# Optimization experiments

Measured on AMD Instinct MI355X. Metric: run time of the kernel, lower is better.

Reference implementation:

```python
import jax, jax.numpy as jnp
import numpy as np

N = 200000
F_IN = 165
H = 128
E = 3200000


def gcn_conv(x, edge_index, W, b):
    # x: [N, Fin], edge_index: [2, E], W: [Fin, Fout], b: [Fout]
    n = x.shape[0]
    h = x @ W  # linear transform first (PyG GCNConv)
    # add self loops
    loops = jnp.arange(n, dtype=edge_index.dtype)
    src = jnp.concatenate([edge_index[0], loops])
    dst = jnp.concatenate([edge_index[1], loops])
    # symmetric normalization: deg computed on dst (in-degree incl. self loops)
    deg = jax.ops.segment_sum(jnp.ones_like(dst, dtype=h.dtype), dst, num_segments=n)
    dinv = jnp.where(deg > 0, jax.lax.rsqrt(deg), 0.0)
    norm = dinv[src] * dinv[dst]  # [E+N]
    msgs = h[src] * norm[:, None]  # gather + scale
    out = jax.ops.segment_sum(msgs, dst, num_segments=n)  # scatter-add
    return out + b


def setup_inputs() -> dict:
    key = jax.random.key(0)
    k = jax.random.split(key, 8)
    x = jax.random.normal(k[0], (N, F_IN), dtype=jnp.float32)
    edge_index = jax.random.randint(k[1], (2, E), 0, N, dtype=jnp.int64)
    s1 = 1.0 / np.sqrt(F_IN)
    s2 = 1.0 / np.sqrt(H)
    W1 = jax.random.uniform(k[2], (F_IN, H), jnp.float32, -s1, s1)
    b1 = jnp.zeros((H,), jnp.float32)
    W2 = jax.random.uniform(k[3], (H, H), jnp.float32, -s2, s2)
    b2 = jnp.zeros((H,), jnp.float32)
    Wl = jax.random.uniform(k[4], (H, 2), jnp.float32, -s2, s2)
    bl = jax.random.uniform(k[5], (2,), jnp.float32, -s2, s2)
    return {"x": x, "edge_index": edge_index, "W1": W1, "b1": b1,
            "W2": W2, "b2": b2, "Wl": Wl, "bl": bl}


def reference(x, edge_index, W1, b1, W2, b2, Wl, bl):
    h = gcn_conv(x, edge_index, W1, b1)
    h = jax.nn.relu(h)
    # dropout p=0.3 is identity in eval mode
    h = gcn_conv(h, edge_index, W2, b2)
    h = jax.nn.relu(h)
    return h @ Wl + bl  # [N, 2]
```

## Files before the change

kernel.cpp:

```cpp
#include <hip/hip_runtime.h>
#include <hip/hip_bf16.h>

#define FIN 165
#define HID 128
#define NPB 256
#define MAXNB 784
#define CAP 4608
#define EPB 4096

typedef __attribute__((ext_vector_type(8))) short short8;
typedef __attribute__((ext_vector_type(4))) float float4v;

__device__ inline unsigned bf16rne(float v) {
    unsigned u = __float_as_uint(v);
    return (u + 0x7fffu + ((u >> 16) & 1u)) >> 16;
}

__device__ inline void bf16split(float v, short& h, short& l) {
    unsigned u = __float_as_uint(v);
    unsigned r = u + 0x7fffu + ((u >> 16) & 1u);
    h = (short)(r >> 16);
    float hf = __uint_as_float(((unsigned)(unsigned short)h) << 16);
    float lf = v - hf;
    unsigned u2 = __float_as_uint(lf);
    unsigned r2 = u2 + 0x7fffu + ((u2 >> 16) & 1u);
    l = (short)(r2 >> 16);
}

__global__ __launch_bounds__(256) void bucket_scatter(const int* __restrict__ src,
                                                      const int* __restrict__ dst,
                                                      int* __restrict__ gcur,
                                                      int2* __restrict__ bucketed,
                                                      int E, int n, int NB) {
    __shared__ int hist[MAXNB];
    __shared__ int base[MAXNB];
    __shared__ int lcur[MAXNB];
    int tid = threadIdx.x;
    long e0 = (long)blockIdx.x * EPB;
    for (int b = tid; b < NB; b += 256) { hist[b] = 0; lcur[b] = 0; }
    __syncthreads();
#pragma unroll
    for (int i = 0; i < EPB / 256; ++i) {
        long e = e0 + i * 256 + tid;
        if (e < E) {
            int d = dst[e], s = src[e];
            if ((unsigned)d < (unsigned)n && (unsigned)s < (unsigned)n)
                atomicAdd(&hist[d >> 8], 1);
        }
    }
    __syncthreads();
    for (int b = tid; b < NB; b += 256) {
        int h = hist[b];
        base[b] = h ? atomicAdd(&gcur[b * 16], h) : 0;
    }
    __syncthreads();
#pragma unroll
    for (int i = 0; i < EPB / 256; ++i) {
        long e = e0 + i * 256 + tid;
        if (e < E) {
            int d = dst[e], s = src[e];
            if ((unsigned)d < (unsigned)n && (unsigned)s < (unsigned)n) {
                int bk = d >> 8;
                int idx = base[bk] + atomicAdd(&lcur[bk], 1);
                if ((unsigned)idx < (unsigned)CAP)
                    bucketed[(size_t)bk * CAP + idx] = make_int2(s, d);
            }
        }
    }
}

__global__ __launch_bounds__(256) void bucket_scan(const int* __restrict__ gcur,
                                                   int* __restrict__ bb, int NB,
                                                   int* __restrict__ rowptr, int n) {
    __shared__ int sm[MAXNB];
    for (int b = threadIdx.x; b < NB; b += 256) sm[b] = gcur[b * 16];
    __syncthreads();
    if (threadIdx.x == 0) {
        int run = 0;
        for (int b = 0; b < NB; ++b) { int c = sm[b]; sm[b] = run; run += c; }
        bb[NB] = run;
        rowptr[n] = run;
    }
    __syncthreads();
    for (int b = threadIdx.x; b < NB; b += 256) bb[b] = sm[b];
}

__global__ __launch_bounds__(256) void build_csr(const int2* __restrict__ bucketed,
                                                 const int* __restrict__ bb,
                                                 float* __restrict__ dinv,
                                                 int* __restrict__ rowptr,
                                                 int* __restrict__ col, int n) {
    __shared__ int deg[NPB];
    __shared__ int scn[NPB];
    __shared__ int cur[NPB];
    int b = blockIdx.x, tid = threadIdx.x;
    int nb0 = b * NPB;
    int ebase = bb[b], cnt = bb[b + 1] - bb[b];
    deg[tid] = 0;
    __syncthreads();
    const int2* ep = bucketed + (size_t)b * CAP;
    for (int i = tid; i < cnt; i += 256) {
        int2 e = ep[i];
        atomicAdd(&deg[e.y - nb0], 1);
    }
    __syncthreads();
    int d = deg[tid];
    scn[tid] = d;
    __syncthreads();
    for (int off = 1; off < 256; off <<= 1) {
        int v = (tid >= off) ? scn[tid - off] : 0;
        __syncthreads();
        scn[tid] += v;
        __syncthreads();
    }
    int excl = scn[tid] - d;
    int node = nb0 + tid;
    if (node < n) {
        dinv[node] = rsqrtf((float)(d + 1));
        rowptr[node] = ebase + excl;
    }
    cur[tid] = excl;
    __syncthreads();
    for (int i = tid; i < cnt; i += 256) {
        int2 e = ep[i];
        int p = atomicAdd(&cur[e.y - nb0], 1);
        col[ebase + p] = e.x;
    }
}

__global__ __launch_bounds__(256) void wswz(const float* __restrict__ W,
                                            short8* __restrict__ out, int K, int k32) {
    int idx = blockIdx.x * 256 + threadIdx.x;
    int tot = k32 * 8 * 64;
    if (idx >= tot) return;
    int lane = idx & 63;
    int ct = (idx >> 6) & 7;
    int ks = idx >> 9;
    int col = ct * 16 + (lane & 15);
    int kb = ks * 32 + (lane >> 4) * 8;
    short8 hi, lo;
#pragma unroll
    for (int j = 0; j < 8; ++j) {
        int k = kb + j;
        float v = (k < K) ? W[k * HID + col] : 0.f;
        short h, l;
        bf16split(v, h, l);
        hi[j] = h; lo[j] = l;
    }
    out[idx] = hi;
    out[tot + idx] = lo;
}

__global__ __launch_bounds__(256) void gemm_mfma(const float* __restrict__ X,
                                                 const short8* __restrict__ Wsw,
                                                 const float* __restrict__ dinv,
                                                 unsigned* __restrict__ H2,
                                                 int n, int K, int kfull, int k32) {
    int wave = threadIdx.x >> 6, lane = threadIdx.x & 63;
    int r0 = blockIdx.x * 64 + wave * 16;
    int m = lane & 15, kph = lane >> 4;
    int row = r0 + m;
    const float* xrow = X + (size_t)row * K + kph * 8;
    const short8* Whi = Wsw;
    const short8* Wlo = Wsw + (size_t)k32 * 8 * 64;

    float4v acc[8];
#pragma unroll
    for (int ct = 0; ct < 8; ++ct) acc[ct] = (float4v){0.f, 0.f, 0.f, 0.f};

    for (int ks = 0; ks < kfull; ++ks) {
        float xv[8];
#pragma unroll
        for (int j = 0; j < 8; ++j) xv[j] = xrow[ks * 32 + j];
        short8 ah, al;
#pragma unroll
        for (int j = 0; j < 8; ++j) {
            short h, l; bf16split(xv[j], h, l);
            ah[j] = h; al[j] = l;
        }
#pragma unroll
        for (int ct = 0; ct < 8; ++ct) {
            short8 bh = Whi[(ks * 8 + ct) * 64 + lane];
            short8 bl = Wlo[(ks * 8 + ct) * 64 + lane];
            acc[ct] = __builtin_amdgcn_mfma_f32_16x16x32_bf16(ah, bh, acc[ct], 0, 0, 0);
            acc[ct] = __builtin_amdgcn_mfma_f32_16x16x32_bf16(al, bh, acc[ct], 0, 0, 0);
            acc[ct] = __builtin_amdgcn_mfma_f32_16x16x32_bf16(ah, bl, acc[ct], 0, 0, 0);
        }
    }
    if (kfull < k32) {
        int ks = kfull;
        int kb = ks * 32 + kph * 8;
        float xv[8];
#pragma unroll
        for (int j = 0; j < 8; ++j) xv[j] = (kb + j < K) ? xrow[ks * 32 + j] : 0.f;
        short8 ah, al;
#pragma unroll
        for (int j = 0; j < 8; ++j) {
            short h, l; bf16split(xv[j], h, l);
            ah[j] = h; al[j] = l;
        }
#pragma unroll
        for (int ct = 0; ct < 8; ++ct) {
            short8 bh = Whi[(ks * 8 + ct) * 64 + lane];
            short8 bl = Wlo[(ks * 8 + ct) * 64 + lane];
            acc[ct] = __builtin_amdgcn_mfma_f32_16x16x32_bf16(ah, bh, acc[ct], 0, 0, 0);
            acc[ct] = __builtin_amdgcn_mfma_f32_16x16x32_bf16(al, bh, acc[ct], 0, 0, 0);
            acc[ct] = __builtin_amdgcn_mfma_f32_16x16x32_bf16(ah, bl, acc[ct], 0, 0, 0);
        }
    }
    int ccol = lane & 15, crow = (lane >> 4) * 4;
    bool evenl = (ccol & 1) == 0;
#pragma unroll
    for (int r = 0; r < 4; ++r) {
        int gr = r0 + crow + r;
        float s = dinv[gr];
#pragma unroll
        for (int ct = 0; ct < 8; ++ct) {
            float v = acc[ct][r] * s;
            float p = __shfl_xor(v, 1);
            if (evenl) {
                unsigned u = bf16rne(v) | (bf16rne(p) << 16);
                H2[(size_t)gr * 64 + ct * 8 + (ccol >> 1)] = u;
            }
        }
    }
}

__device__ inline void bf2_unpack(unsigned u, float& f0, float& f1) {
    f0 = __uint_as_float(u << 16);
    f1 = __uint_as_float(u & 0xffff0000u);
}

__global__ __launch_bounds__(256) void agg_relu(const unsigned* __restrict__ HS2,
                                                const int* __restrict__ rowptr,
                                                const int* __restrict__ col,
                                                const float* __restrict__ dinv,
                                                const float* __restrict__ bias,
                                                float* __restrict__ Y, int n) {
    int node = blockIdx.x * 4 + (threadIdx.x >> 6);
    int lane = threadIdx.x & 63;
    if (node >= n) return;
    int start = rowptr[node], end = rowptr[node + 1];
    float2 acc;
    {
        float f0, f1;
        bf2_unpack(HS2[(size_t)node * 64 + lane], f0, f1);
        acc.x = f0; acc.y = f1;
    }
    for (int j0 = start; j0 < end; j0 += 64) {
        int cnt = min(64, end - j0);
        int cv = (j0 + lane < end) ? col[j0 + lane] : 0;
        int t = 0;
        for (; t + 8 <= cnt; t += 8) {
            unsigned uv[8];
#pragma unroll
            for (int q = 0; q < 8; ++q) {
                int c = __shfl(cv, t + q);
                uv[q] = HS2[(size_t)c * 64 + lane];
            }
#pragma unroll
            for (int q = 0; q < 8; ++q) {
                float f0, f1; bf2_unpack(uv[q], f0, f1);
                acc.x += f0; acc.y += f1;
            }
        }
        for (; t < cnt; ++t) {
            int c = __shfl(cv, t);
            float f0, f1; bf2_unpack(HS2[(size_t)c * 64 + lane], f0, f1);
            acc.x += f0; acc.y += f1;
        }
    }
    float s = dinv[node];
    float2 b = *(const float2*)&bias[2 * lane];
    float2 o;
    o.x = fmaxf(acc.x * s + b.x, 0.f);
    o.y = fmaxf(acc.y * s + b.y, 0.f);
    *(float2*)&Y[(long)node * HID + 2 * lane] = o;
}

__global__ __launch_bounds__(256) void agg_relu_head(const unsigned* __restrict__ HS2,
                                                     const int* __restrict__ rowptr,
                                                     const int* __restrict__ col,
                                                     const float* __restrict__ dinv,
                                                     const float* __restrict__ bias,
                                                     const float* __restrict__ Wl,
                                                     const float* __restrict__ bl,
                                                     float* __restrict__ out, int n) {
    int node = blockIdx.x * 4 + (threadIdx.x >> 6);
    int lane = threadIdx.x & 63;
    if (node >= n) return;
    int start = rowptr[node], end = rowptr[node + 1];
    float2 acc;
    {
        float f0, f1;
        bf2_unpack(HS2[(size_t)node * 64 + lane], f0, f1);
        acc.x = f0; acc.y = f1;
    }
    for (int j0 = start; j0 < end; j0 += 64) {
        int cnt = min(64, end - j0);
        int cv = (j0 + lane < end) ? col[j0 + lane] : 0;
        int t = 0;
        for (; t + 8 <= cnt; t += 8) {
            unsigned uv[8];
#pragma unroll
            for (int q = 0; q < 8; ++q) {
                int c = __shfl(cv, t + q);
                uv[q] = HS2[(size_t)c * 64 + lane];
            }
#pragma unroll
            for (int q = 0; q < 8; ++q) {
                float f0, f1; bf2_unpack(uv[q], f0, f1);
                acc.x += f0; acc.y += f1;
            }
        }
        for (; t < cnt; ++t) {
            int c = __shfl(cv, t);
            float f0, f1; bf2_unpack(HS2[(size_t)c * 64 + lane], f0, f1);
            acc.x += f0; acc.y += f1;
        }
    }
    float s = dinv[node];
    float2 b = *(const float2*)&bias[2 * lane];
    float vx = fmaxf(acc.x * s + b.x, 0.f);
    float vy = fmaxf(acc.y * s + b.y, 0.f);
    float4 wl = *(const float4*)&Wl[4 * lane];
    float a0 = vx * wl.x + vy * wl.z;
    float a1 = vx * wl.y + vy * wl.w;
#pragma unroll
    for (int off = 32; off > 0; off >>= 1) {
        a0 += __shfl_xor(a0, off);
        a1 += __shfl_xor(a1, off);
    }
    if (lane == 0) {
        out[node * 2 + 0] = a0 + bl[0];
        out[node * 2 + 1] = a1 + bl[1];
    }
}

extern "C" void kernel_launch(void* const* d_in, const int* in_sizes, int n_in,
                              void* d_out, int out_size, void* d_ws, size_t ws_size,
                              hipStream_t stream) {
    const float* x  = (const float*)d_in[0];
    const int*   ei = (const int*)d_in[1];
    const float* W1 = (const float*)d_in[2];
    const float* b1 = (const float*)d_in[3];
    const float* W2 = (const float*)d_in[4];
    const float* b2 = (const float*)d_in[5];
    const float* Wl = (const float*)d_in[6];
    const float* bl = (const float*)d_in[7];
    float* out = (float*)d_out;

    int n = in_sizes[0] / FIN;
    int E = in_sizes[1] / 2;
    int NB = (n + NPB - 1) / NPB;
    const int* srcp = ei;
    const int* dstp = ei + E;

    char* w = (char*)d_ws;
    auto alloc = [&](size_t bytes) {
        char* p = w;
        w += (bytes + 255) & ~(size_t)255;
        return (void*)p;
    };
    int*      gcur    = (int*)     alloc((size_t)NB * 16 * 4);
    int*      bb      = (int*)     alloc(((size_t)NB + 1) * 4);
    int*      rowptr  = (int*)     alloc(((size_t)n + 1) * 4);
    float*    dinv    = (float*)   alloc((size_t)n * 4);
    int*      colv    = (int*)     alloc((size_t)E * 4);
    unsigned* hbuf    = (unsigned*)alloc((size_t)n * 64 * 4);
    float*    ybuf    = (float*)   alloc((size_t)n * HID * 4);
    const int K32_1 = (FIN + 31) / 32;
    const int K32_2 = HID / 32;
    short8*   w1sw    = (short8*)  alloc((size_t)2 * K32_1 * 8 * 64 * 16);
    short8*   w2sw    = (short8*)  alloc((size_t)2 * K32_2 * 8 * 64 * 16);
    int2*     bucketed = (int2*)ybuf;

    hipMemsetAsync(gcur, 0, (size_t)NB * 16 * 4, stream);

    wswz<<<(K32_1 * 8 * 64 + 255) / 256, 256, 0, stream>>>(W1, w1sw, FIN, K32_1);
    wswz<<<(K32_2 * 8 * 64 + 255) / 256, 256, 0, stream>>>(W2, w2sw, HID, K32_2);

    bucket_scatter<<<(E + EPB - 1) / EPB, 256, 0, stream>>>(srcp, dstp, gcur,
                                                            bucketed, E, n, NB);
    bucket_scan<<<1, 256, 0, stream>>>(gcur, bb, NB, rowptr, n);
    build_csr<<<NB, 256, 0, stream>>>(bucketed, bb, dinv, rowptr, colv, n);

    gemm_mfma<<<n / 64, 256, 0, stream>>>(x, w1sw, dinv, hbuf, n, FIN, FIN / 32, K32_1);
    agg_relu<<<(n + 3) / 4, 256, 0, stream>>>(hbuf, rowptr, colv, dinv, b1, ybuf, n);

    gemm_mfma<<<n / 64, 256, 0, stream>>>(ybuf, w2sw, dinv, hbuf, n, HID, HID / 32, K32_2);

    agg_relu_head<<<(n + 3) / 4, 256, 0, stream>>>(hbuf, rowptr, colv, dinv, b2,
                                                   Wl, bl, out, n);
}
```

Measured before the change: 725.2 us.

## Fuse layer-1 aggregation with layer-2 GEMM through shared-memory tile

Replaces the separate layer-1 aggregation kernel and the second GEMM with one kernel. Each wave aggregates 16 nodes and stages their ReLU outputs in LDS, and the block then runs the split-bf16 MFMA GEMM on that 64-row tile before writing bf16 H2. This removes the full fp32 intermediate write and re-read through global memory, and one kernel launch. In exchange, each wave walks its nodes serially and the 33KB LDS tile limits occupancy, so there is less parallelism to hide gather latency. The bucketed scratch now aliases hbuf instead of the dropped ybuf.

```diff
diff --git a/kernel.cpp b/kernel.cpp
--- a/kernel.cpp
+++ b/kernel.cpp
@@ -25,6 +25,11 @@
     unsigned u2 = __float_as_uint(lf);
     unsigned r2 = u2 + 0x7fffu + ((u2 >> 16) & 1u);
     l = (short)(r2 >> 16);
+}
+
+__device__ inline void bf2_unpack(unsigned u, float& f0, float& f1) {
+    f0 = __uint_as_float(u << 16);
+    f1 = __uint_as_float(u & 0xffff0000u);
 }
 
 __global__ __launch_bounds__(256) void bucket_scatter(const int* __restrict__ src,
@@ -226,56 +231,100 @@
     }
 }
 
-__device__ inline void bf2_unpack(unsigned u, float& f0, float& f1) {
-    f0 = __uint_as_float(u << 16);
-    f1 = __uint_as_float(u & 0xffff0000u);
-}
-
-__global__ __launch_bounds__(256) void agg_relu(const unsigned* __restrict__ HS2,
+__global__ __launch_bounds__(256) void agg_gemm(const unsigned* __restrict__ HS2,
                                                 const int* __restrict__ rowptr,
                                                 const int* __restrict__ col,
                                                 const float* __restrict__ dinv,
                                                 const float* __restrict__ bias,
-                                                float* __restrict__ Y, int n) {
-    int node = blockIdx.x * 4 + (threadIdx.x >> 6);
-    int lane = threadIdx.x & 63;
-    if (node >= n) return;
-    int start = rowptr[node], end = rowptr[node + 1];
-    float2 acc;
-    {
-        float f0, f1;
-        bf2_unpack(HS2[(size_t)node * 64 + lane], f0, f1);
-        acc.x = f0; acc.y = f1;
-    }
-    for (int j0 = start; j0 < end; j0 += 64) {
-        int cnt = min(64, end - j0);
-        int cv = (j0 + lane < end) ? col[j0 + lane] : 0;
-        int t = 0;
-        for (; t + 8 <= cnt; t += 8) {
-            unsigned uv[8];
-#pragma unroll
-            for (int q = 0; q < 8; ++q) {
-                int c = __shfl(cv, t + q);
-                uv[q] = HS2[(size_t)c * 64 + lane];
-            }
-#pragma unroll
-            for (int q = 0; q < 8; ++q) {
-                float f0, f1; bf2_unpack(uv[q], f0, f1);
+                                                const short8* __restrict__ Wsw,
+                                                unsigned* __restrict__ H2o,
+                                                int n, int k32) {
+    __shared__ float yt[64][130];
+    int wave = threadIdx.x >> 6, lane = threadIdx.x & 63;
+    int r0 = blockIdx.x * 64 + wave * 16;
+    float2 bv = *(const float2*)&bias[2 * lane];
+
+    for (int i = 0; i < 16; ++i) {
+        int node = r0 + i;
+        int start = rowptr[node], end = rowptr[node + 1];
+        float2 acc;
+        {
+            float f0, f1;
+            bf2_unpack(HS2[(size_t)node * 64 + lane], f0, f1);
+            acc.x = f0; acc.y = f1;
+        }
+        for (int j0 = start; j0 < end; j0 += 64) {
+            int cnt = min(64, end - j0);
+            int cv = (j0 + lane < end) ? col[j0 + lane] : 0;
+            int t = 0;
+            for (; t + 8 <= cnt; t += 8) {
+                unsigned uv[8];
+#pragma unroll
+                for (int q = 0; q < 8; ++q) {
+                    int c = __shfl(cv, t + q);
+                    uv[q] = HS2[(size_t)c * 64 + lane];
+                }
+#pragma unroll
+                for (int q = 0; q < 8; ++q) {
+                    float f0, f1; bf2_unpack(uv[q], f0, f1);
+                    acc.x += f0; acc.y += f1;
+                }
+            }
+            for (; t < cnt; ++t) {
+                int c = __shfl(cv, t);
+                float f0, f1; bf2_unpack(HS2[(size_t)c * 64 + lane], f0, f1);
                 acc.x += f0; acc.y += f1;
             }
         }
-        for (; t < cnt; ++t) {
-            int c = __shfl(cv, t);
-            float f0, f1; bf2_unpack(HS2[(size_t)c * 64 + lane], f0, f1);
-            acc.x += f0; acc.y += f1;
-        }
-    }
-    float s = dinv[node];
-    float2 b = *(const float2*)&bias[2 * lane];
-    float2 o;
-    o.x = fmaxf(acc.x * s + b.x, 0.f);
-    o.y = fmaxf(acc.y * s + b.y, 0.f);
-    *(float2*)&Y[(long)node * HID + 2 * lane] = o;
+        float s = dinv[node];
+        float2 o;
+        o.x = fmaxf(acc.x * s + bv.x, 0.f);
+        o.y = fmaxf(acc.y * s + bv.y, 0.f);
+        *(float2*)&yt[wave * 16 + i][2 * lane] = o;
+    }
+
+    int m = lane & 15, kph = lane >> 4;
+    const short8* Whi = Wsw;
+    const short8* Wlo = Wsw + (size_t)k32 * 8 * 64;
+    float4v acc[8];
+#pragma unroll
+    for (int ct = 0; ct < 8; ++ct) acc[ct] = (float4v){0.f, 0.f, 0.f, 0.f};
+#pragma unroll
+    for (int ks = 0; ks < 4; ++ks) {
+        float xv[8];
+#pragma unroll
+        for (int j = 0; j < 8; ++j) xv[j] = yt[wave * 16 + m][ks * 32 + kph * 8 + j];
+        short8 ah, al;
+#pragma unroll
+        for (int j = 0; j < 8; ++j) {
+            short h, l; bf16split(xv[j], h, l);
+            ah[j] = h; al[j] = l;
+        }
+#pragma unroll
+        for (int ct = 0; ct < 8; ++ct) {
+            short8 bh = Whi[(ks * 8 + ct) * 64 + lane];
+            short8 bl = Wlo[(ks * 8 + ct) * 64 + lane];
+            acc[ct] = __builtin_amdgcn_mfma_f32_16x16x32_bf16(ah, bh, acc[ct], 0, 0, 0);
+            acc[ct] = __builtin_amdgcn_mfma_f32_16x16x32_bf16(al, bh, acc[ct], 0, 0, 0);
+            acc[ct] = __builtin_amdgcn_mfma_f32_16x16x32_bf16(ah, bl, acc[ct], 0, 0, 0);
+        }
+    }
+    int ccol = lane & 15, crow = (lane >> 4) * 4;
+    bool evenl = (ccol & 1) == 0;
+#pragma unroll
+    for (int r = 0; r < 4; ++r) {
+        int gr = r0 + crow + r;
+        float s = dinv[gr];
+#pragma unroll
+        for (int ct = 0; ct < 8; ++ct) {
+            float v = acc[ct][r] * s;
+            float p = __shfl_xor(v, 1);
+            if (evenl) {
+                unsigned u = bf16rne(v) | (bf16rne(p) << 16);
+                H2o[(size_t)gr * 64 + ct * 8 + (ccol >> 1)] = u;
+            }
+        }
+    }
 }
 
 __global__ __launch_bounds__(256) void agg_relu_head(const unsigned* __restrict__ HS2,
@@ -368,12 +417,12 @@
     float*    dinv    = (float*)   alloc((size_t)n * 4);
     int*      colv    = (int*)     alloc((size_t)E * 4);
     unsigned* hbuf    = (unsigned*)alloc((size_t)n * 64 * 4);
-    float*    ybuf    = (float*)   alloc((size_t)n * HID * 4);
+    unsigned* h2buf   = (unsigned*)alloc((size_t)n * 64 * 4);
     const int K32_1 = (FIN + 31) / 32;
     const int K32_2 = HID / 32;
     short8*   w1sw    = (short8*)  alloc((size_t)2 * K32_1 * 8 * 64 * 16);
     short8*   w2sw    = (short8*)  alloc((size_t)2 * K32_2 * 8 * 64 * 16);
-    int2*     bucketed = (int2*)ybuf;
+    int2*     bucketed = (int2*)hbuf;
 
     hipMemsetAsync(gcur, 0, (size_t)NB * 16 * 4, stream);
 
@@ -386,10 +435,10 @@
     build_csr<<<NB, 256, 0, stream>>>(bucketed, bb, dinv, rowptr, colv, n);
 
     gemm_mfma<<<n / 64, 256, 0, stream>>>(x, w1sw, dinv, hbuf, n, FIN, FIN / 32, K32_1);
-    agg_relu<<<(n + 3) / 4, 256, 0, stream>>>(hbuf, rowptr, colv, dinv, b1, ybuf, n);
-
-    gemm_mfma<<<n / 64, 256, 0, stream>>>(ybuf, w2sw, dinv, hbuf, n, HID, HID / 32, K32_2);
-
-    agg_relu_head<<<(n + 3) / 4, 256, 0, stream>>>(hbuf, rowptr, colv, dinv, b2,
+
+    agg_gemm<<<n / 64, 256, 0, stream>>>(hbuf, rowptr, colv, dinv, b1, w2sw,
+                                         h2buf, n, K32_2);
+
+    agg_relu_head<<<(n + 3) / 4, 256, 0, stream>>>(h2buf, rowptr, colv, dinv, b2,
                                                    Wl, bl, out, n);
 }
```

Measured after the change: 755.2 us. 1.04x slower.

## Split aggregation into two feature-half passes over a half-split H layout

Applied to the files above, without the earlier changes.

The GEMM now writes H as two separate feature halves, each an n×64 bf16 plane. Each aggregation runs as two passes, one per half, so every gather touches a 25.6 MB working set that may fit in the last-level cache rather than the full 51 MB table. The head kernel adds the second pass onto the partial result of the first, and a separate buffer is added for the second layer's H. The cost is reading the CSR twice and making per-lane 2-byte gathers instead of 4-byte ones.

```diff
diff --git a/kernel.cpp b/kernel.cpp
--- a/kernel.cpp
+++ b/kernel.cpp
@@ -25,6 +25,10 @@
     unsigned u2 = __float_as_uint(lf);
     unsigned r2 = u2 + 0x7fffu + ((u2 >> 16) & 1u);
     l = (short)(r2 >> 16);
+}
+
+__device__ inline float bf16tof(unsigned short us) {
+    return __uint_as_float(((unsigned)us) << 16);
 }
 
 __global__ __launch_bounds__(256) void bucket_scatter(const int* __restrict__ src,
@@ -220,120 +224,101 @@
             float p = __shfl_xor(v, 1);
             if (evenl) {
                 unsigned u = bf16rne(v) | (bf16rne(p) << 16);
-                H2[(size_t)gr * 64 + ct * 8 + (ccol >> 1)] = u;
+                H2[(size_t)(ct >> 2) * n * 32 + (size_t)gr * 32
+                   + (ct & 3) * 8 + (ccol >> 1)] = u;
             }
         }
     }
 }
 
-__device__ inline void bf2_unpack(unsigned u, float& f0, float& f1) {
-    f0 = __uint_as_float(u << 16);
-    f1 = __uint_as_float(u & 0xffff0000u);
-}
-
-__global__ __launch_bounds__(256) void agg_relu(const unsigned* __restrict__ HS2,
-                                                const int* __restrict__ rowptr,
-                                                const int* __restrict__ col,
-                                                const float* __restrict__ dinv,
-                                                const float* __restrict__ bias,
-                                                float* __restrict__ Y, int n) {
+__global__ __launch_bounds__(256) void agg_pass_y(const unsigned* __restrict__ HS2,
+                                                  const int* __restrict__ rowptr,
+                                                  const int* __restrict__ col,
+                                                  const float* __restrict__ dinv,
+                                                  const float* __restrict__ bias,
+                                                  float* __restrict__ Y,
+                                                  int n, int p) {
     int node = blockIdx.x * 4 + (threadIdx.x >> 6);
     int lane = threadIdx.x & 63;
     if (node >= n) return;
+    const unsigned short* Hp = (const unsigned short*)(HS2 + (size_t)p * n * 32);
     int start = rowptr[node], end = rowptr[node + 1];
-    float2 acc;
-    {
-        float f0, f1;
-        bf2_unpack(HS2[(size_t)node * 64 + lane], f0, f1);
-        acc.x = f0; acc.y = f1;
-    }
+    float acc = bf16tof(Hp[(size_t)node * 64 + lane]);
     for (int j0 = start; j0 < end; j0 += 64) {
         int cnt = min(64, end - j0);
         int cv = (j0 + lane < end) ? col[j0 + lane] : 0;
         int t = 0;
         for (; t + 8 <= cnt; t += 8) {
-            unsigned uv[8];
+            unsigned short uv[8];
 #pragma unroll
             for (int q = 0; q < 8; ++q) {
                 int c = __shfl(cv, t + q);
-                uv[q] = HS2[(size_t)c * 64 + lane];
+                uv[q] = Hp[(size_t)c * 64 + lane];
             }
 #pragma unroll
-            for (int q = 0; q < 8; ++q) {
-                float f0, f1; bf2_unpack(uv[q], f0, f1);
-                acc.x += f0; acc.y += f1;
-            }
+            for (int q = 0; q < 8; ++q) acc += bf16tof(uv[q]);
         }
         for (; t < cnt; ++t) {
             int c = __shfl(cv, t);
-            float f0, f1; bf2_unpack(HS2[(size_t)c * 64 + lane], f0, f1);
-            acc.x += f0; acc.y += f1;
-        }
-    }
-    float s = dinv[node];
-    float2 b = *(const float2*)&bias[2 * lane];
-    float2 o;
-    o.x = fmaxf(acc.x * s + b.x, 0.f);
-    o.y = fmaxf(acc.y * s + b.y, 0.f);
-    *(float2*)&Y[(long)node * HID + 2 * lane] = o;
-}
-
-__global__ __launch_bounds__(256) void agg_relu_head(const unsigned* __restrict__ HS2,
+            acc += bf16tof(Hp[(size_t)c * 64 + lane]);
+        }
+    }
+    float v = acc * dinv[node] + bias[p * 64 + lane];
+    Y[(size_t)node * HID + p * 64 + lane] = fmaxf(v, 0.f);
+}
+
+__global__ __launch_bounds__(256) void agg_pass_head(const unsigned* __restrict__ HS2,
                                                      const int* __restrict__ rowptr,
                                                      const int* __restrict__ col,
                                                      const float* __restrict__ dinv,
                                                      const float* __restrict__ bias,
                                                      const float* __restrict__ Wl,
                                                      const float* __restrict__ bl,
-                                                     float* __restrict__ out, int n) {
+                                                     float* __restrict__ out,
+                                                     int n, int p) {
     int node = blockIdx.x * 4 + (threadIdx.x >> 6);
     int lane = threadIdx.x & 63;
     if (node >= n) return;
+    const unsigned short* Hp = (const unsigned short*)(HS2 + (size_t)p * n * 32);
     int start = rowptr[node], end = rowptr[node + 1];
-    float2 acc;
-    {
-        float f0, f1;
-        bf2_unpack(HS2[(size_t)node * 64 + lane], f0, f1);
-        acc.x = f0; acc.y = f1;
-    }
+    float acc = bf16tof(Hp[(size_t)node * 64 + lane]);
     for (int j0 = start; j0 < end; j0 += 64) {
         int cnt = min(64, end - j0);
         int cv = (j0 + lane < end) ? col[j0 + lane] : 0;
         int t = 0;
         for (; t + 8 <= cnt; t += 8) {
-            unsigned uv[8];
+            unsigned short uv[8];
 #pragma unroll
             for (int q = 0; q < 8; ++q) {
                 int c = __shfl(cv, t + q);
-                uv[q] = HS2[(size_t)c * 64 + lane];
+                uv[q] = Hp[(size_t)c * 64 + lane];
             }
 #pragma unroll
-            for (int q = 0; q < 8; ++q) {
-                float f0, f1; bf2_unpack(uv[q], f0, f1);
-                acc.x += f0; acc.y += f1;
-            }
+            for (int q = 0; q < 8; ++q) acc += bf16tof(uv[q]);
         }
         for (; t < cnt; ++t) {
             int c = __shfl(cv, t);
-            float f0, f1; bf2_unpack(HS2[(size_t)c * 64 + lane], f0, f1);
-            acc.x += f0; acc.y += f1;
-        }
-    }
-    float s = dinv[node];
-    float2 b = *(const float2*)&bias[2 * lane];
-    float vx = fmaxf(acc.x * s + b.x, 0.f);
-    float vy = fmaxf(acc.y * s + b.y, 0.f);
-    float4 wl = *(const float4*)&Wl[4 * lane];
-    float a0 = vx * wl.x + vy * wl.z;
-    float a1 = vx * wl.y + vy * wl.w;
+            acc += bf16tof(Hp[(size_t)c * 64 + lane]);
+        }
+    }
+    int f = p * 64 + lane;
+    float vx = fmaxf(acc * dinv[node] + bias[f], 0.f);
+    float2 wl = *(const float2*)&Wl[2 * f];
+    float a0 = vx * wl.x;
+    float a1 = vx * wl.y;
 #pragma unroll
     for (int off = 32; off > 0; off >>= 1) {
         a0 += __shfl_xor(a0, off);
         a1 += __shfl_xor(a1, off);
     }
     if (lane == 0) {
-        out[node * 2 + 0] = a0 + bl[0];
-        out[node * 2 + 1] = a1 + bl[1];
+        if (p == 0) {
+            out[node * 2 + 0] = a0;
+            out[node * 2 + 1] = a1;
+        } else {
+            out[node * 2 + 0] = out[node * 2 + 0] + a0 + bl[0];
+            out[node * 2 + 1] = out[node * 2 + 1] + a1 + bl[1];
+        }
     }
 }
 
@@ -368,6 +353,7 @@
     float*    dinv    = (float*)   alloc((size_t)n * 4);
     int*      colv    = (int*)     alloc((size_t)E * 4);
     unsigned* hbuf    = (unsigned*)alloc((size_t)n * 64 * 4);
+    unsigned* h2buf   = (unsigned*)alloc((size_t)n * 64 * 4);
     float*    ybuf    = (float*)   alloc((size_t)n * HID * 4);
     const int K32_1 = (FIN + 31) / 32;
     const int K32_2 = HID / 32;
@@ -386,10 +372,14 @@
     build_csr<<<NB, 256, 0, stream>>>(bucketed, bb, dinv, rowptr, colv, n);
 
     gemm_mfma<<<n / 64, 256, 0, stream>>>(x, w1sw, dinv, hbuf, n, FIN, FIN / 32, K32_1);
-    agg_relu<<<(n + 3) / 4, 256, 0, stream>>>(hbuf, rowptr, colv, dinv, b1, ybuf, n);
-
-    gemm_mfma<<<n / 64, 256, 0, stream>>>(ybuf, w2sw, dinv, hbuf, n, HID, HID / 32, K32_2);
-
-    agg_relu_head<<<(n + 3) / 4, 256, 0, stream>>>(hbuf, rowptr, colv, dinv, b2,
-                                                   Wl, bl, out, n);
-}
+
+    agg_pass_y<<<(n + 3) / 4, 256, 0, stream>>>(hbuf, rowptr, colv, dinv, b1, ybuf, n, 0);
+    agg_pass_y<<<(n + 3) / 4, 256, 0, stream>>>(hbuf, rowptr, colv, dinv, b1, ybuf, n, 1);
+
+    gemm_mfma<<<n / 64, 256, 0, stream>>>(ybuf, w2sw, dinv, h2buf, n, HID, HID / 32, K32_2);
+
+    agg_pass_head<<<(n + 3) / 4, 256, 0, stream>>>(h2buf, rowptr, colv, dinv, b2,
+                                                   Wl, bl, out, n, 0);
+    agg_pass_head<<<(n + 3) / 4, 256, 0, stream>>>(h2buf, rowptr, colv, dinv, b2,
+                                                   Wl, bl, out, n, 1);
+}
```

Result: slower. 899.5 us (+24.0%).
